# Kernel tuning notes

Measured on AMD Instinct MI355X. Metric: run time of the kernel, lower is better.

## Reference

```python
import jax, jax.numpy as jnp
import numpy as np

CHUNK_SIZE = 2048
LOCAL_WINDOW = 384
CHUNK_LEN = CHUNK_SIZE - LOCAL_WINDOW  # 1664
N_HEADS = 16
N_KV_HEADS = 4
HEAD_DIM = 128
HIDDEN = 2048
SEQ = 3 * CHUNK_LEN  # 4992
NEG_INF = -1e9


def _cos_sin(positions, dim=HEAD_DIM, base=10000.0):
    inv = 1.0 / (base ** (np.arange(0, dim, 2, dtype=np.float64) / dim))
    freqs = np.outer(np.asarray(positions, np.float64), inv)
    emb = np.concatenate([freqs, freqs], axis=-1)
    return jnp.asarray(np.cos(emb), jnp.float32), jnp.asarray(np.sin(emb), jnp.float32)


def setup_inputs() -> dict:
    key = jax.random.key(0)
    ks = jax.random.split(key, 5)
    hidden_states = jax.random.normal(ks[0], (1, SEQ, HIDDEN), jnp.float32) * 0.02
    position_ids = jnp.arange(SEQ, dtype=jnp.int32)[None, :]
    q_cos, q_sin = _cos_sin(np.arange(SEQ))                 # intra rotary (positions mod chunk_len)
    qc_cos, qc_sin = _cos_sin(np.arange(SEQ) + CHUNK_LEN)   # cross-chunk rotary variant
    k_cos, k_sin = _cos_sin(np.arange(SEQ))                 # key rotary (absolute positions)
    kv_dim = N_KV_HEADS * HEAD_DIM
    Wq = jax.random.normal(ks[1], (N_HEADS * HEAD_DIM, HIDDEN), jnp.float32) * 0.02
    Wk = jax.random.normal(ks[2], (kv_dim, HIDDEN), jnp.float32) * 0.02
    Wv = jax.random.normal(ks[3], (kv_dim, HIDDEN), jnp.float32) * 0.02
    Wo = jax.random.normal(ks[4], (HIDDEN, N_HEADS * HEAD_DIM), jnp.float32) * 0.02
    return dict(hidden_states=hidden_states, position_ids=position_ids,
                q_cos=q_cos, q_sin=q_sin, qc_cos=qc_cos, qc_sin=qc_sin,
                k_cos=k_cos, k_sin=k_sin, Wq=Wq, Wk=Wk, Wv=Wv, Wo=Wo)


def _rotate_half(x):
    x1, x2 = jnp.split(x, 2, axis=-1)
    return jnp.concatenate([-x2, x1], axis=-1)


def _rope(x, cos_t, sin_t, pid):
    # x: [b,h,s,d], pid: [b,s] -> cos/sin [b,1,s,d]
    cos = cos_t[pid][:, None]
    sin = sin_t[pid][:, None]
    return x * cos + _rotate_half(x) * sin


def _attn(q, k, v, causal):
    # flash-attn semantics: scale = head_dim**-0.5, returns output and fp32 LSE [b,h,q]
    scale = q.shape[-1] ** -0.5
    s = jnp.einsum('bhqd,bhkd->bhqk', q, k).astype(jnp.float32) * scale
    if causal:
        L, K = s.shape[-2], s.shape[-1]
        mask = jnp.tril(jnp.ones((L, K), bool))
        s = jnp.where(mask, s, NEG_INF)
    lse = jax.nn.logsumexp(s, axis=-1)
    p = jax.nn.softmax(s, axis=-1).astype(q.dtype)
    out = jnp.einsum('bhqk,bhkd->bhqd', p, v)
    return out, lse


def _merge(parts):
    # LSE-weighted merge of partial attention outputs (weights detached, as in torch)
    outs = jnp.stack([p[0] for p in parts])       # [n,b,h,q,d]
    lses = jnp.stack([p[1] for p in parts])       # [n,b,h,q] fp32
    w = jax.lax.stop_gradient(jax.nn.softmax(lses, axis=0))
    return jnp.sum(outs * w[..., None].astype(outs.dtype), axis=0)


def _forward(hidden_states, position_ids, q_cos, q_sin, qc_cos, qc_sin, k_cos, k_sin, Wq, Wk, Wv, Wo):
    b, s, _ = hidden_states.shape
    q = (hidden_states @ Wq.T).reshape(b, s, N_HEADS, HEAD_DIM).transpose(0, 2, 1, 3)
    k = (hidden_states @ Wk.T).reshape(b, s, N_KV_HEADS, HEAD_DIM).transpose(0, 2, 1, 3)
    v = (hidden_states @ Wv.T).reshape(b, s, N_KV_HEADS, HEAD_DIM).transpose(0, 2, 1, 3)

    k = _rope(k, k_cos, k_sin, position_ids)
    pid = position_ids % CHUNK_LEN

    groups = N_HEADS // N_KV_HEADS
    k = jnp.repeat(k, groups, axis=1)
    v = jnp.repeat(v, groups, axis=1)

    n_chunks = s // CHUNK_LEN
    # chunk 0: intra causal only
    q0 = _rope(q[:, :, :CHUNK_LEN], q_cos, q_sin, pid[:, :CHUNK_LEN])
    out0, _ = _attn(q0, k[:, :, :CHUNK_LEN], v[:, :, :CHUNK_LEN], causal=True)
    outs = [out0]
    for i in range(1, n_chunks):
        b0 = i * CHUNK_LEN
        e = b0 + CHUNK_LEN
        qi = q[:, :, b0:e]
        pid_c = pid[:, b0:e]
        parts = [_attn(_rope(qi, q_cos, q_sin, pid_c), k[:, :, b0:e], v[:, :, b0:e], causal=True),
                 _attn(_rope(qi, qc_cos, qc_sin, pid_c), k[:, :, b0 - CHUNK_LEN:b0], v[:, :, b0 - CHUNK_LEN:b0], causal=False)]
        if b0 - CHUNK_LEN > 0:
            pid_i = jnp.full_like(pid_c, CHUNK_LEN - 1)
            parts.append(_attn(_rope(qi, qc_cos, qc_sin, pid_i), k[:, :, :b0 - CHUNK_LEN], v[:, :, :b0 - CHUNK_LEN], causal=False))
        outs.append(_merge(parts))
    attn_out = jnp.concatenate(outs, axis=2)                      # [b,h,s,d]
    attn_out = attn_out.transpose(0, 2, 1, 3).reshape(b, s, -1)   # [b,s,h*d]
    return attn_out @ Wo.T


def reference(hidden_states, position_ids, q_cos, q_sin, qc_cos, qc_sin, k_cos, k_sin, Wq, Wk, Wv, Wo):
    return _forward(hidden_states, position_ids, q_cos, q_sin, qc_cos, qc_sin, k_cos, k_sin, Wq, Wk, Wv, Wo)
```

## Files before the change

kernel.cpp:

```cpp
#include <hip/hip_runtime.h>

typedef unsigned short u16;
typedef unsigned int u32;
typedef __attribute__((ext_vector_type(8))) __bf16 bf16x8;
typedef __attribute__((ext_vector_type(4))) float f32x4;
typedef __attribute__((ext_vector_type(16))) float f32x16;

#define CLEN 1664
#define SEQL 4992
#define NHEADS 16
#define HD 128
#define HID 2048
#define KVD 512
#define SCALE 0.08838834764831845f
#define QPARTS 84

__device__ __forceinline__ u16 f2bf(float f) {
  union { float f; u32 u; } v; v.f = f;
  u32 u = v.u;
  return (u16)((u + 0x7FFFu + ((u >> 16) & 1u)) >> 16);
}
__device__ __forceinline__ float bf2f(u16 h) {
  union { u32 u; float f; } v; v.u = (u32)h << 16;
  return v.f;
}
__device__ __forceinline__ f32x4 mfma16(bf16x8 a, bf16x8 b, f32x4 c) {
  return __builtin_amdgcn_mfma_f32_16x16x32_bf16(a, b, c, 0, 0, 0);
}
__device__ __forceinline__ f32x16 mfma32(bf16x8 a, bf16x8 b, f32x16 c) {
  return __builtin_amdgcn_mfma_f32_32x32x16_bf16(a, b, c, 0, 0, 0);
}
__device__ __forceinline__ u32 cvtpk(float lo, float hi) {
  u32 r;
  asm("v_cvt_pk_bf16_f32 %0, %1, %2" : "=v"(r) : "v"(lo), "v"(hi));
  return r;
}
__device__ __forceinline__ void gload_lds16(const u16* g, u16* l) {
  __builtin_amdgcn_global_load_lds((const __attribute__((address_space(1))) void*)g,
                                   (__attribute__((address_space(3))) void*)l, 16, 0, 0);
}

#define CVT_Q0 2555904
#define CVT_Q1 1048576
#define CVT_Q2 262144
#define CVT_Q3 262144
#define CVT_Q4 1048576
__device__ __forceinline__ void cvt4(const float* s, u16* d, int q) {
  float4 v = *(const float4*)(s + (size_t)q * 4);
  uint2 p;
  p.x = (u32)f2bf(v.x) | ((u32)f2bf(v.y) << 16);
  p.y = (u32)f2bf(v.z) | ((u32)f2bf(v.w) << 16);
  *(uint2*)(d + (size_t)q * 4) = p;
}
__global__ void cvt_all_kernel(const float* __restrict__ hidden, const float* __restrict__ Wq,
                               const float* __restrict__ Wk, const float* __restrict__ Wv,
                               const float* __restrict__ Wo, u16* __restrict__ h_bf,
                               u16* __restrict__ Wqkv, u16* __restrict__ Wo_bf,
                               u32* __restrict__ cnt) {
  int q = blockIdx.x * blockDim.x + threadIdx.x;
  if (q < 8) cnt[q * 64] = 0;
  if (q < CVT_Q0) { cvt4(hidden, h_bf, q); return; }
  q -= CVT_Q0;
  if (q < CVT_Q1) { cvt4(Wq, Wqkv, q); return; }
  q -= CVT_Q1;
  if (q < CVT_Q2) { cvt4(Wk, Wqkv + 2048 * 2048, q); return; }
  q -= CVT_Q2;
  if (q < CVT_Q3) { cvt4(Wv, Wqkv + 2560 * 2048, q); return; }
  q -= CVT_Q3;
  if (q < CVT_Q4) cvt4(Wo, Wo_bf, q);
}

#define RP_N0 1277952
#define RP_N1 851968
#define RP_N2 425984
#define RP_N3 319488
__device__ __forceinline__ void rope8(const u16* __restrict__ src, u16* __restrict__ dst,
                                      const float* __restrict__ ctab, const float* __restrict__ stab,
                                      int s, int dstrow, int col, int rowlen, int pid, float scl) {
  const int dh = col & 127;
  const bool hih = dh >= 64;
  const u16* rowp = src + (size_t)s * rowlen;
  union { uint4 u; u16 h[8]; } X, P, O;
  X.u = *(const uint4*)(rowp + col);
  P.u = *(const uint4*)(rowp + col + (hih ? -64 : 64));
  const float* cp = ctab + pid * 128 + dh;
  const float* sp = stab + pid * 128 + dh;
#pragma unroll
  for (int j = 0; j < 8; ++j) {
    float v = bf2f(X.h[j]) * cp[j] + (hih ? bf2f(P.h[j]) : -bf2f(P.h[j])) * sp[j];
    O.h[j] = f2bf(v * scl);
  }
  *(uint4*)(dst + (size_t)dstrow * rowlen + col) = O.u;
}
__global__ void rope_all_kernel(const u16* __restrict__ q_tmp, const u16* __restrict__ k_tmp,
                                u16* __restrict__ qa, u16* __restrict__ qb, u16* __restrict__ qf,
                                u16* __restrict__ k_bf, const float* __restrict__ q_cos,
                                const float* __restrict__ q_sin, const float* __restrict__ qc_cos,
                                const float* __restrict__ qc_sin, const float* __restrict__ k_cos,
                                const float* __restrict__ k_sin) {
  int o = blockIdx.x * blockDim.x + threadIdx.x;
  if (o < RP_N0) {
    int r = o >> 8, col = (o & 255) * 8;
    rope8(q_tmp, qa, q_cos, q_sin, r, r, col, 2048, r % CLEN, SCALE);
    return;
  }
  o -= RP_N0;
  if (o < RP_N1) {
    int r = o >> 8, col = (o & 255) * 8, s = CLEN + r;
    rope8(q_tmp, qb, qc_cos, qc_sin, s, r, col, 2048, s % CLEN, SCALE);
    return;
  }
  o -= RP_N1;
  if (o < RP_N2) {
    int r = o >> 8, col = (o & 255) * 8, s = 2 * CLEN + r;
    rope8(q_tmp, qf, qc_cos, qc_sin, s, r, col, 2048, CLEN - 1, SCALE);
    return;
  }
  o -= RP_N2;
  if (o < RP_N3) {
    int r = o >> 6, col = (o & 63) * 8;
    rope8(k_tmp, k_bf, k_cos, k_sin, r, r, col, 512, r, 1.0f);
  }
}

__global__ __launch_bounds__(256) void gemm_qkv(const u16* __restrict__ A, const u16* __restrict__ B,
                                                u16* __restrict__ q_tmp, u16* __restrict__ k_tmp,
                                                u16* __restrict__ vT) {
  __shared__ __align__(16) u16 Al[128 * 64];
  __shared__ __align__(16) u16 Bl[128 * 64];
  const int K = HID;
  const int t = threadIdx.x;
  const int lane = t & 63, wid = t >> 6;
  const int g = lane >> 4, c = lane & 15;
  const int wr = wid >> 1, wc = wid & 1;
  const int bid = blockIdx.x;
  const int wg = (bid & 7) * 117 + (bid >> 3);
  const int m0 = (wg % 39) * 128, n0 = (wg / 39) * 128;

  f32x4 acc[4][4];
#pragma unroll
  for (int m = 0; m < 4; ++m)
#pragma unroll
    for (int n = 0; n < 4; ++n) acc[m][n] = (f32x4){0.f, 0.f, 0.f, 0.f};

  const int scol = (t & 7) * 8;
  for (int k0 = 0; k0 < K; k0 += 64) {
    __syncthreads();
#pragma unroll
    for (int i = 0; i < 4; ++i) {
      const int r = i * 32 + (t >> 3);
      gload_lds16(A + (size_t)(m0 + r) * K + k0 + scol, Al + i * 2048 + wid * 512);
      gload_lds16(B + (size_t)(n0 + r) * K + k0 + scol, Bl + i * 2048 + wid * 512);
    }
    __syncthreads();
#pragma unroll
    for (int kk = 0; kk < 2; ++kk) {
      bf16x8 af[4], bfr[4];
#pragma unroll
      for (int m = 0; m < 4; ++m)
        af[m] = *(const bf16x8*)(Al + (wr * 64 + m * 16 + c) * 64 + kk * 32 + g * 8);
#pragma unroll
      for (int n = 0; n < 4; ++n)
        bfr[n] = *(const bf16x8*)(Bl + (wc * 64 + n * 16 + c) * 64 + kk * 32 + g * 8);
#pragma unroll
      for (int m = 0; m < 4; ++m)
#pragma unroll
        for (int n = 0; n < 4; ++n)
          acc[m][n] = mfma16(af[m], bfr[n], acc[m][n]);
    }
  }
#pragma unroll
  for (int m = 0; m < 4; ++m)
#pragma unroll
    for (int n = 0; n < 4; ++n)
#pragma unroll
      for (int j = 0; j < 4; ++j) {
        const int row = m0 + wr * 64 + m * 16 + 4 * g + j;
        const int col = n0 + wc * 64 + n * 16 + c;
        const float v = acc[m][n][j];
        if (n0 < 2048)       q_tmp[(size_t)row * 2048 + col] = f2bf(v);
        else if (n0 < 2560)  k_tmp[(size_t)row * 512 + (col - 2048)] = f2bf(v);
        else                 vT[(size_t)(col - 2560) * SEQL + row] = f2bf(v);
      }
}

__global__ __launch_bounds__(256) void gemm_o(const u16* __restrict__ A, const u16* __restrict__ B,
                                              float* __restrict__ Cf) {
  __shared__ __align__(16) u16 Al[128 * 64];
  __shared__ __align__(16) u16 Bl[128 * 64];
  const int K = HID, N = HID;
  const int t = threadIdx.x;
  const int lane = t & 63, wid = t >> 6;
  const int g = lane >> 4, c = lane & 15;
  const int wr = wid >> 1, wc = wid & 1;
  const int bid = blockIdx.x;
  const int wg = (bid & 7) * 78 + (bid >> 3);
  const int m0 = (wg % 39) * 128, n0 = (wg / 39) * 128;

  f32x4 acc[4][4];
#pragma unroll
  for (int m = 0; m < 4; ++m)
#pragma unroll
    for (int n = 0; n < 4; ++n) acc[m][n] = (f32x4){0.f, 0.f, 0.f, 0.f};

  const int scol = (t & 7) * 8;
  for (int k0 = 0; k0 < K; k0 += 64) {
    __syncthreads();
#pragma unroll
    for (int i = 0; i < 4; ++i) {
      const int r = i * 32 + (t >> 3);
      gload_lds16(A + (size_t)(m0 + r) * K + k0 + scol, Al + i * 2048 + wid * 512);
      gload_lds16(B + (size_t)(n0 + r) * K + k0 + scol, Bl + i * 2048 + wid * 512);
    }
    __syncthreads();
#pragma unroll
    for (int kk = 0; kk < 2; ++kk) {
      bf16x8 af[4], bfr[4];
#pragma unroll
      for (int m = 0; m < 4; ++m)
        af[m] = *(const bf16x8*)(Al + (wr * 64 + m * 16 + c) * 64 + kk * 32 + g * 8);
#pragma unroll
      for (int n = 0; n < 4; ++n)
        bfr[n] = *(const bf16x8*)(Bl + (wc * 64 + n * 16 + c) * 64 + kk * 32 + g * 8);
#pragma unroll
      for (int m = 0; m < 4; ++m)
#pragma unroll
        for (int n = 0; n < 4; ++n)
          acc[m][n] = mfma16(af[m], bfr[n], acc[m][n]);
    }
  }
#pragma unroll
  for (int m = 0; m < 4; ++m)
#pragma unroll
    for (int n = 0; n < 4; ++n)
#pragma unroll
      for (int j = 0; j < 4; ++j) {
        const int row = m0 + wr * 64 + m * 16 + 4 * g + j;
        const int col = n0 + wc * 64 + n * 16 + c;
        Cf[(size_t)row * N + col] = acc[m][n][j];
      }
}

__global__ __launch_bounds__(512, 4) void attn_kernel(
    const u16* __restrict__ qa, const u16* __restrict__ qbuf, const u16* __restrict__ qf,
    const u16* __restrict__ kbf, const u16* __restrict__ vT,
    u16* __restrict__ Opart, float* __restrict__ lseout, u32* __restrict__ cnt) {
  __shared__ __align__(16) u16 smem[2 * 16384];
  __shared__ int wsh;

  const int t = threadIdx.x, wid = t >> 6, lane = t & 63;
  const int ql = lane & 31, hi = lane >> 5;
  const int qid = blockIdx.x & 7;
  const int kvh = qid >> 1, headpar = qid & 1;
  const int ksr = t >> 4, ksc = t & 15;
  const int vsr = t >> 3, vsc = t & 7;

  for (;;) {
    __syncthreads();
    if (t == 0) wsh = (int)atomicAdd(cnt + qid * 64, 1u);
    __syncthreads();
    const int w = wsh;
    if (w >= QPARTS) break;

    const int head = kvh * 4 + ((w & 1) << 1) + headpar;
    const int rk = w >> 1;
    int chunk, seg, qb;
    if (rk < 21) {
      const int part = rk / 7; qb = rk % 7;
      chunk = (part == 0) ? 1 : 2;
      seg = (part == 2) ? 1 : 0;
    } else if (rk < 24) {
      chunk = rk - 21; seg = chunk; qb = 6;
    } else {
      const int g2 = rk - 24;
      qb = 5 - g2 / 3; chunk = g2 % 3; seg = chunk;
    }
    const bool causal = (seg == chunk);
    const int nt = causal ? ((qb == 6) ? 26 : (4 * qb + 4)) : 26;
    const int slot = causal ? 0 : ((chunk - seg == 1) ? 1 : 2);
    const int kvbase = seg * CLEN;
    const int qcb = qb * 256 + wid * 32;
    const int qpos = qcb + ql;
    const bool wact = qcb < CLEN;

    const u16* qp; int qoff;
    if (causal)                { qp = qa;   qoff = 0; }
    else if (chunk - seg == 1) { qp = qbuf; qoff = CLEN; }
    else                       { qp = qf;   qoff = 2 * CLEN; }

    bf16x8 aq[8];
    {
      const int qrow = wact ? (chunk * CLEN + qpos - qoff) : 0;
      const u16* qptr = qp + (size_t)qrow * HID + head * HD + hi * 8;
#pragma unroll
      for (int ck = 0; ck < 8; ++ck) aq[ck] = *(const bf16x8*)(qptr + ck * 16);
    }

    float l_r = 0.f;
    f32x16 oacc[4];
#pragma unroll
    for (int db = 0; db < 4; ++db)
#pragma unroll
      for (int r = 0; r < 16; ++r) oacc[db][r] = 0.f;

    auto stage = [&](int b, int kt) {
      const int kv0 = kt * 64;
#pragma unroll
      for (int i = 0; i < 2; ++i) {
        const int rr = ksr + 32 * i;
        const int gs = ksc ^ (rr & 7);
        gload_lds16(kbf + (size_t)(kvbase + kv0 + rr) * KVD + kvh * HD + gs * 8,
                    smem + b * 16384 + i * 4096 + wid * 512);
      }
#pragma unroll
      for (int i = 0; i < 2; ++i) {
        const int rr = vsr + 64 * i;
        const int gs = vsc ^ (rr & 7);
        gload_lds16(vT + (size_t)(kvh * HD + rr) * SEQL + kvbase + kv0 + gs * 8,
                    smem + b * 16384 + 8192 + i * 4096 + wid * 512);
      }
    };

    stage(0, 0);
    int cur = 0;
    for (int kt = 0; kt < nt; ++kt) {
      if (kt + 1 < nt) {
        stage(cur ^ 1, kt + 1);
        asm volatile("s_waitcnt vmcnt(4)" ::: "memory");
      } else {
        asm volatile("s_waitcnt vmcnt(0)" ::: "memory");
      }
      __builtin_amdgcn_s_barrier();
      const int kv0 = kt * 64;
      const u16* Kb = smem + cur * 16384;
      const u16* Vb = smem + cur * 16384 + 8192;
#pragma unroll
      for (int s = 0; s < 2; ++s) {
        if (wact && !(causal && kv0 + 32 * s > qcb + 31)) {
          f32x16 sacc;
#pragma unroll
          for (int r = 0; r < 16; ++r) sacc[r] = 0.f;
          const int kr = 32 * s + ql;
          const int r7 = lane & 7;
#pragma unroll
          for (int ck = 0; ck < 8; ++ck) {
            bf16x8 kb = *(const bf16x8*)(Kb + kr * 128 + (((2 * ck + hi) ^ r7) * 8));
            sacc = mfma32(kb, aq[ck], sacc);
          }
          float e[16];
          float rs = 0.f;
#pragma unroll
          for (int r = 0; r < 16; ++r) {
            const int kvp = kv0 + 32 * s + (r & 3) + 8 * (r >> 2) + 4 * hi;
            float ev = sacc[r];
            if (causal && kvp > qpos) ev = -1e30f;
            e[r] = __expf(ev);
            rs += e[r];
          }
          rs += __shfl_xor(rs, 32);
          l_r += rs;
          u32 wp[8];
#pragma unroll
          for (int j = 0; j < 8; ++j) wp[j] = cvtpk(e[2 * j], e[2 * j + 1]);
#pragma unroll
          for (int ks = 0; ks < 2; ++ks) {
            union { uint4 u; bf16x8 v; } pa;
            pa.u.x = wp[4 * ks]; pa.u.y = wp[4 * ks + 1];
            pa.u.z = wp[4 * ks + 2]; pa.u.w = wp[4 * ks + 3];
            const int g4a = 8 * s + 4 * ks + hi;
            const int sw = (lane & 7) << 1;
#pragma unroll
            for (int db = 0; db < 4; ++db) {
              const int vrow = 32 * db + ql;
              const uint2 v0 = *(const uint2*)(Vb + vrow * 64 + ((g4a ^ sw) * 4));
              const uint2 v1 = *(const uint2*)(Vb + vrow * 64 + (((g4a + 2) ^ sw) * 4));
              union { uint4 u; bf16x8 v; } bv;
              bv.u.x = v0.x; bv.u.y = v0.y; bv.u.z = v1.x; bv.u.w = v1.y;
              oacc[db] = mfma32(pa.v, bv.v, oacc[db]);
            }
          }
        }
      }
      __builtin_amdgcn_s_barrier();
      cur ^= 1;
    }
    if (wact) {
      const float linv = 1.0f / l_r;
      u16* scr = smem + wid * 4096;
#pragma unroll
      for (int r = 0; r < 16; ++r) {
        const int rrow = (r & 3) + 8 * (r >> 2) + 4 * hi;
        const float li = __shfl(linv, rrow);
#pragma unroll
        for (int db = 0; db < 4; ++db)
          scr[rrow * 128 + db * 32 + ql] = f2bf(oacc[db][r] * li);
      }
      asm volatile("s_waitcnt lgkmcnt(0)" ::: "memory");
      const int rcol = lane & 15;
#pragma unroll
      for (int p = 0; p < 8; ++p) {
        const int row = p * 4 + (lane >> 4);
        uint4 v = *(const uint4*)(scr + row * 128 + rcol * 8);
        const size_t grow = (size_t)(chunk * CLEN + qcb + row);
        *(uint4*)(Opart + ((size_t)slot * SEQL + grow) * HID + head * HD + rcol * 8) = v;
      }
      if (hi == 0)
        lseout[((size_t)slot * NHEADS + head) * SEQL + chunk * CLEN + qcb + ql] = __logf(l_r);
    }
  }
}

__global__ void merge_kernel(const u16* __restrict__ Opart, const float* __restrict__ lse,
                             u16* __restrict__ amrg) {
  const int idx = blockIdx.x * blockDim.x + threadIdx.x;
  const int row = idx >> 8;
  const int col = (idx & 255) * 8;
  const int head = col >> 7;
  const int np = row / CLEN + 1;
  float ls[3];
  float mx = -1e30f;
  for (int i = 0; i < np; ++i) {
    ls[i] = lse[((size_t)i * NHEADS + head) * SEQL + row];
    mx = fmaxf(mx, ls[i]);
  }
  float wsum = 0.f;
  for (int i = 0; i < np; ++i) { ls[i] = __expf(ls[i] - mx); wsum += ls[i]; }
  const float inv = 1.0f / wsum;
  float acc[8];
#pragma unroll
  for (int j = 0; j < 8; ++j) acc[j] = 0.f;
  for (int i = 0; i < np; ++i) {
    union { uint4 u; u16 h[8]; } X;
    X.u = *(const uint4*)(Opart + ((size_t)i * SEQL + row) * (size_t)HID + col);
#pragma unroll
    for (int j = 0; j < 8; ++j) acc[j] += ls[i] * bf2f(X.h[j]);
  }
  union { uint4 u; u16 h[8]; } O;
#pragma unroll
  for (int j = 0; j < 8; ++j) O.h[j] = f2bf(acc[j] * inv);
  *(uint4*)(amrg + (size_t)row * 2048 + col) = O.u;
}

extern "C" void kernel_launch(void* const* d_in, const int* in_sizes, int n_in,
                              void* d_out, int out_size, void* d_ws, size_t ws_size,
                              hipStream_t stream) {
  (void)in_sizes; (void)n_in; (void)out_size; (void)ws_size;
  const float* hidden = (const float*)d_in[0];
  const float* q_cos = (const float*)d_in[2];
  const float* q_sin = (const float*)d_in[3];
  const float* qc_cos = (const float*)d_in[4];
  const float* qc_sin = (const float*)d_in[5];
  const float* k_cos = (const float*)d_in[6];
  const float* k_sin = (const float*)d_in[7];
  const float* Wq = (const float*)d_in[8];
  const float* Wk = (const float*)d_in[9];
  const float* Wv = (const float*)d_in[10];
  const float* Wo = (const float*)d_in[11];
  float* out = (float*)d_out;

  char* ws = (char*)d_ws;
  u16* Wo_bf = (u16*)(ws + 0);
  u16* qa    = (u16*)(ws + 8388608);
  u16* qb    = (u16*)(ws + 28835840);
  u16* qf    = (u16*)(ws + 42467328);
  u16* k_bf  = (u16*)(ws + 49283072);
  u16* vT    = (u16*)(ws + 54394880);
  char* BIG  = ws + 59506688;
  u16* h_bf  = (u16*)(BIG + 0);
  u16* Wqkv  = (u16*)(BIG + 20447232);
  u16* q_tmp = (u16*)(BIG + 33030144);
  u16* k_tmp = (u16*)(BIG + 53477376);
  u16* Opart = (u16*)(BIG + 0);
  float* lse = (float*)(BIG + 61341696);
  u32* cnt   = (u32*)(BIG + 61341696 + 958464);
  u16* amrg  = qa;

  cvt_all_kernel<<<dim3(20224), dim3(256), 0, stream>>>(hidden, Wq, Wk, Wv, Wo, h_bf, Wqkv, Wo_bf, cnt);
  gemm_qkv<<<dim3(936), 256, 0, stream>>>(h_bf, Wqkv, q_tmp, k_tmp, vT);
  rope_all_kernel<<<dim3(11232), dim3(256), 0, stream>>>(q_tmp, k_tmp, qa, qb, qf, k_bf,
                                                         q_cos, q_sin, qc_cos, qc_sin, k_cos, k_sin);
  attn_kernel<<<dim3(512), dim3(512), 0, stream>>>(qa, qb, qf, k_bf, vT, Opart, lse, cnt);
  merge_kernel<<<dim3(SEQL), dim3(256), 0, stream>>>(Opart, lse, amrg);
  gemm_o<<<dim3(624), 256, 0, stream>>>(amrg, Wo_bf, out);
}
```

Baseline: 573.1 us.

## Use exp2 with log2e-prescaled queries, two-queue work scheduler, and MFMA priority hints

Folds log2(e) into the query scaling applied during RoPE so the attention inner loop can use the hardware exp2 instruction instead of expf. Simplifies the causal mask to one threshold compare per element. Adds s_setprio around the MFMA blocks and splits the atomic work counter into a heavy queue and a small queue, so long items are dispatched first for better load balance. This relies on the LSE output being consistent with the log2-domain scores.

Measured after the change: 577.8 us. No clear change (+0.8%).

```diff
diff --git a/kernel.cpp b/kernel.cpp
--- a/kernel.cpp
+++ b/kernel.cpp
@@ -13,7 +13,9 @@
 #define HID 2048
 #define KVD 512
 #define SCALE 0.08838834764831845f
-#define QPARTS 84
+#define SCLOG2E 0.12752615142058843f
+#define NHEAVY 48
+#define NSMALL 36
 
 __device__ __forceinline__ u16 f2bf(float f) {
   union { float f; u32 u; } v; v.f = f;
@@ -33,6 +35,11 @@
 __device__ __forceinline__ u32 cvtpk(float lo, float hi) {
   u32 r;
   asm("v_cvt_pk_bf16_f32 %0, %1, %2" : "=v"(r) : "v"(lo), "v"(hi));
+  return r;
+}
+__device__ __forceinline__ float exp2v(float x) {
+  float r;
+  asm("v_exp_f32 %0, %1" : "=v"(r) : "v"(x));
   return r;
 }
 __device__ __forceinline__ void gload_lds16(const u16* g, u16* l) {
@@ -58,7 +65,7 @@
                                u16* __restrict__ Wqkv, u16* __restrict__ Wo_bf,
                                u32* __restrict__ cnt) {
   int q = blockIdx.x * blockDim.x + threadIdx.x;
-  if (q < 8) cnt[q * 64] = 0;
+  if (q < 8) { cnt[q * 64] = 0; cnt[q * 64 + 1] = 0; }
   if (q < CVT_Q0) { cvt4(hidden, h_bf, q); return; }
   q -= CVT_Q0;
   if (q < CVT_Q1) { cvt4(Wq, Wqkv, q); return; }
@@ -101,19 +108,19 @@
   int o = blockIdx.x * blockDim.x + threadIdx.x;
   if (o < RP_N0) {
     int r = o >> 8, col = (o & 255) * 8;
-    rope8(q_tmp, qa, q_cos, q_sin, r, r, col, 2048, r % CLEN, SCALE);
+    rope8(q_tmp, qa, q_cos, q_sin, r, r, col, 2048, r % CLEN, SCLOG2E);
     return;
   }
   o -= RP_N0;
   if (o < RP_N1) {
     int r = o >> 8, col = (o & 255) * 8, s = CLEN + r;
-    rope8(q_tmp, qb, qc_cos, qc_sin, s, r, col, 2048, s % CLEN, SCALE);
+    rope8(q_tmp, qb, qc_cos, qc_sin, s, r, col, 2048, s % CLEN, SCLOG2E);
     return;
   }
   o -= RP_N1;
   if (o < RP_N2) {
     int r = o >> 8, col = (o & 255) * 8, s = 2 * CLEN + r;
-    rope8(q_tmp, qf, qc_cos, qc_sin, s, r, col, 2048, CLEN - 1, SCALE);
+    rope8(q_tmp, qf, qc_cos, qc_sin, s, r, col, 2048, CLEN - 1, SCLOG2E);
     return;
   }
   o -= RP_N2;
@@ -257,10 +264,17 @@
 
   for (;;) {
     __syncthreads();
-    if (t == 0) wsh = (int)atomicAdd(cnt + qid * 64, 1u);
+    if (t == 0) {
+      int h = (int)atomicAdd(cnt + qid * 64, 1u);
+      if (h >= NHEAVY) {
+        int s2 = (int)atomicAdd(cnt + qid * 64 + 1, 1u);
+        h = (s2 < NSMALL) ? (NHEAVY + s2) : -1;
+      }
+      wsh = h;
+    }
     __syncthreads();
     const int w = wsh;
-    if (w >= QPARTS) break;
+    if (w < 0) break;
 
     const int head = kvh * 4 + ((w & 1) << 1) + headpar;
     const int rk = w >> 1;
@@ -342,19 +356,21 @@
           for (int r = 0; r < 16; ++r) sacc[r] = 0.f;
           const int kr = 32 * s + ql;
           const int r7 = lane & 7;
+          __builtin_amdgcn_s_setprio(1);
 #pragma unroll
           for (int ck = 0; ck < 8; ++ck) {
             bf16x8 kb = *(const bf16x8*)(Kb + kr * 128 + (((2 * ck + hi) ^ r7) * 8));
             sacc = mfma32(kb, aq[ck], sacc);
           }
+          __builtin_amdgcn_s_setprio(0);
+          const int thr = qpos - kv0 - 32 * s - 4 * hi;
           float e[16];
           float rs = 0.f;
 #pragma unroll
           for (int r = 0; r < 16; ++r) {
-            const int kvp = kv0 + 32 * s + (r & 3) + 8 * (r >> 2) + 4 * hi;
-            float ev = sacc[r];
-            if (causal && kvp > qpos) ev = -1e30f;
-            e[r] = __expf(ev);
+            const int crow_r = (r & 3) + 8 * (r >> 2);
+            float ev = (causal && crow_r > thr) ? -1e30f : sacc[r];
+            e[r] = exp2v(ev);
             rs += e[r];
           }
           rs += __shfl_xor(rs, 32);
@@ -362,6 +378,7 @@
           u32 wp[8];
 #pragma unroll
           for (int j = 0; j < 8; ++j) wp[j] = cvtpk(e[2 * j], e[2 * j + 1]);
+          __builtin_amdgcn_s_setprio(1);
 #pragma unroll
           for (int ks = 0; ks < 2; ++ks) {
             union { uint4 u; bf16x8 v; } pa;
@@ -379,6 +396,7 @@
               oacc[db] = mfma32(pa.v, bv.v, oacc[db]);
             }
           }
+          __builtin_amdgcn_s_setprio(0);
         }
       }
       __builtin_amdgcn_s_barrier();
```
